# Optimization experiments

Measured on AMD Instinct MI355X. Metric: run time of the kernel, lower is better.

## Reference

```python
import jax, jax.numpy as jnp
import numpy as np

N = 200_000   # total nodes across batched AIGs
E = 400_000   # edges (fan-in ~2 per gate)
D = 64        # input_dim == dim_hidden (required by in-place scatter in _gru_forward)
B = 16        # number of graphs in batch
LF = 12       # num forward topological levels
LB = 12       # num backward topological levels
NUM_ROUNDS = 1


def setup_inputs() -> dict:
    key = jax.random.key(0)
    ks = jax.random.split(key, 9)
    node_type = jax.random.randint(ks[0], (N,), 0, 3, dtype=jnp.int32)
    num_inverted_predecessors = jax.random.randint(ks[1], (N,), 0, 3, dtype=jnp.int32)
    edge_index = jax.random.randint(ks[2], (2, E), 0, N, dtype=jnp.int32)
    forward_level = jax.random.randint(ks[3], (N,), 0, LF, dtype=jnp.int32)
    backward_level = jax.random.randint(ks[4], (N,), 0, LB, dtype=jnp.int32)
    batch = jnp.sort(jax.random.randint(ks[5], (N,), 0, B, dtype=jnp.int32))
    s = 1.0 / np.sqrt(D)
    W_enc = jax.random.normal(ks[6], (2, D), dtype=jnp.float32) * 0.5
    b_enc = jnp.zeros((D,), dtype=jnp.float32)
    W_f = jax.random.normal(ks[7], (D, D), dtype=jnp.float32) * s
    b_f = jnp.zeros((D,), dtype=jnp.float32)
    W_b = jax.random.normal(ks[8], (D, D), dtype=jnp.float32) * s
    b_b = jnp.zeros((D,), dtype=jnp.float32)
    return dict(node_type=node_type,
                num_inverted_predecessors=num_inverted_predecessors,
                edge_index=edge_index,
                forward_level=forward_level,
                backward_level=backward_level,
                batch=batch,
                W_enc=W_enc, b_enc=b_enc,
                W_f=W_f, b_f=b_f,
                W_b=W_b, b_b=b_b)


def reference(node_type, num_inverted_predecessors, edge_index,
              forward_level, backward_level, batch,
              W_enc, b_enc, W_f, b_f, W_b, b_b):
    # h_init = node_encoder(cat(node_type, num_inverted_predecessors))
    x = jnp.stack([node_type, num_inverted_predecessors], axis=1).astype(W_enc.dtype)  # [N,2]
    h = x @ W_enc + b_enc  # [N,D] node_state
    src, dst = edge_index[0], edge_index[1]

    for _ in range(NUM_ROUNDS):
        # forward topological sweep: level l nodes receive sum of mlp(h_src)
        # over incoming edges whose destination is at level l (subgraph dim=1).
        for l in range(1, LF):
            m = h @ W_f + b_f                                    # AggConv mlp on current state
            e_w = (forward_level[dst] == l).astype(h.dtype)      # edges into level-l nodes
            msg = jax.ops.segment_sum(m[src] * e_w[:, None], dst, num_segments=N)
            h = jnp.where((forward_level == l)[:, None], msg, h)  # scatter l_msg into node_state
        # backward sweep (reverse flow): level-l sources receive sum of
        # mlp_b(h_dst) over outgoing edges (subgraph dim=0, target_to_source).
        for l in range(1, LB):
            m = h @ W_b + b_b
            e_w = (backward_level[src] == l).astype(h.dtype)
            msg = jax.ops.segment_sum(m[dst] * e_w[:, None], src, num_segments=N)
            h = jnp.where((backward_level == l)[:, None], msg, h)

    # readout over output nodes (node_type == 1): [global_max_pool, global_add_pool]
    out_mask = (node_type == 1)
    neg_inf = jnp.finfo(h.dtype).min
    max_pool = jax.ops.segment_max(jnp.where(out_mask[:, None], h, neg_inf), batch, num_segments=B)
    sum_pool = jax.ops.segment_sum(h * out_mask[:, None].astype(h.dtype), batch, num_segments=B)
    return jnp.concatenate([max_pool, sum_pool], axis=1)  # [B, 2*D]
```

## Files before the change

### kernel.cpp

```cpp
#include <hip/hip_runtime.h>
#include <float.h>

#define NLVL 12
#define NB   16
#define NBLK 256
#define EBLK 2048
#define SWBLK 1024


struct Params {
    const int *nt, *ninv, *src, *dst, *fl, *bl, *batch;
    const float *We, *be, *Wf, *bf, *Wb, *bb;
    float *hN, *hB, *tabg, *out;
    int *rowptr, *cursor, *col, *nb_f, *nb_b, *onodes, *bsums, *meta, *plarr, *bar;
    int *cntf, *cntb, *cnto, *blkf, *blkb, *blko;
    int N, E, M, outN;
};

__device__ __forceinline__ float rlanef(float x, int l) {
    return __int_as_float(__builtin_amdgcn_readlane(__float_as_int(x), l));
}
__device__ __forceinline__ void sti(int* a, int v) {
    __hip_atomic_store(a, v, __ATOMIC_RELAXED, __HIP_MEMORY_SCOPE_AGENT);
}
__device__ __forceinline__ void stf(float* a, float v) {
    __hip_atomic_store(a, v, __ATOMIC_RELAXED, __HIP_MEMORY_SCOPE_AGENT);
}
__device__ __forceinline__ int ald(int* a) {
    return __hip_atomic_load(a, __ATOMIC_RELAXED, __HIP_MEMORY_SCOPE_AGENT);
}
__device__ __forceinline__ int afa(int* a, int v) {
    return __hip_atomic_fetch_add(a, v, __ATOMIC_RELAXED, __HIP_MEMORY_SCOPE_AGENT);
}

__device__ __forceinline__ void gbar3(int* bar, int nblk, int t) {
    __syncthreads();
    if (threadIdx.x == 0) {
        const int line = blockIdx.x & 15;
        const int per  = nblk >> 4;
        int a = afa(&bar[line * 32], 1);
        if (a == per * t - 1) {
            int m = afa(&bar[16 * 32], 1);
            if (m == 16 * t - 1) {
                sti(&bar[17 * 32], t);
            } else {
                while (ald(&bar[17 * 32]) < t) __builtin_amdgcn_s_sleep(1);
            }
            for (int b = line; b < nblk; b += 16)
                sti(&bar[(18 + b) * 32], t);
        } else {
            while (ald(&bar[(18 + blockIdx.x) * 32]) < t) __builtin_amdgcn_s_sleep(4);
        }
    }
    asm volatile("" ::: "memory");
    __syncthreads();
}

__global__ void k_edge_deg(Params p) {
    int g = blockIdx.x * 256 + threadIdx.x, gs = gridDim.x * 256;
    for (int e = g; e < p.E; e += gs) {
        atomicAdd(&p.rowptr[p.dst[e]], 1);
        atomicAdd(&p.rowptr[p.N + p.src[e]], 1);
    }
}

__global__ void k_deg_hist(Params p) {
    __shared__ int hf[NLVL], hb[NLVL], ho[NB];
    int tid = threadIdx.x, bid = blockIdx.x;
    if (tid < NLVL) { hf[tid] = 0; hb[tid] = 0; }
    if (tid < NB) ho[tid] = 0;
    __syncthreads();
    int chunk = (p.N + gridDim.x - 1) / gridDim.x;
    int lo = bid * chunk, hi = lo + chunk; if (hi > p.N) hi = p.N;
    for (int i = lo + tid; i < hi; i += 256) {
        int f = p.fl[i], b = p.bl[i];
        int t = p.nt[i], iv = p.ninv[i];
        p.plarr[i] = f | (b << 4) | ((t * 3 + iv) << 8);
        atomicAdd(&hf[f], 1);
        atomicAdd(&hb[b], 1);
        if (t == 1) atomicAdd(&ho[p.batch[i]], 1);
    }
    __syncthreads();
    if (tid < NLVL) { p.cntf[tid * NBLK + bid] = hf[tid]; p.cntb[tid * NBLK + bid] = hb[tid]; }
    if (tid < NB) p.cnto[tid * NBLK + bid] = ho[tid];
}

__global__ void k_scan1(int* __restrict__ data, int M, int* __restrict__ bsums) {
    __shared__ int s[512];
    int t = threadIdx.x;
    int g = blockIdx.x * 512 + t;
    int v = (g < M) ? data[g] : 0;
    s[t] = v;
    __syncthreads();
    for (int off = 1; off < 512; off <<= 1) {
        int add = (t >= off) ? s[t - off] : 0;
        __syncthreads();
        s[t] += add;
        __syncthreads();
    }
    if (g < M) data[g] = s[t] - v;
    if (t == 511) bsums[blockIdx.x] = s[511];
}

__global__ void k_scan_top(int* __restrict__ bsums, int nblk, Params p,
                           float* __restrict__ out, int outN) {
    __shared__ int s[1024];
    __shared__ int tot[48];
    int t = threadIdx.x;
    int* meta = p.meta;
    for (int i = t; i < outN; i += 1024)
        out[i] = ((i & 127) < 64) ? -FLT_MAX : 0.0f;
    if (t < 576) {
        int row = t >> 6, j = t & 63;
        float nf = (float)(row / 3), iv = (float)(row % 3);
        p.tabg[t] = fmaf(nf, p.We[j], fmaf(iv, p.We[64 + j], p.be[j]));
    }
    int seg = t >> 8, b = t & 255;
    for (int r = 0; r < 3; r++) {
        int l = 4 * r + seg;
        int v = p.cntf[l * NBLK + b];
        s[t] = v; __syncthreads();
        for (int off = 1; off < NBLK; off <<= 1) {
            int add = (b >= off) ? s[t - off] : 0; __syncthreads();
            s[t] += add; __syncthreads();
        }
        p.blkf[l * NBLK + b] = s[t] - v;
        if (b == NBLK - 1) tot[l] = s[t];
        __syncthreads();
    }
    for (int r = 0; r < 3; r++) {
        int l = 4 * r + seg;
        int v = p.cntb[l * NBLK + b];
        s[t] = v; __syncthreads();
        for (int off = 1; off < NBLK; off <<= 1) {
            int add = (b >= off) ? s[t - off] : 0; __syncthreads();
            s[t] += add; __syncthreads();
        }
        p.blkb[l * NBLK + b] = s[t] - v;
        if (b == NBLK - 1) tot[16 + l] = s[t];
        __syncthreads();
    }
    for (int r = 0; r < 4; r++) {
        int l = 4 * r + seg;
        int v = p.cnto[l * NBLK + b];
        s[t] = v; __syncthreads();
        for (int off = 1; off < NBLK; off <<= 1) {
            int add = (b >= off) ? s[t - off] : 0; __syncthreads();
            s[t] += add; __syncthreads();
        }
        p.blko[l * NBLK + b] = s[t] - v;
        if (b == NBLK - 1) tot[32 + l] = s[t];
        __syncthreads();
    }
    if (t == 0) { int a = 0; for (int l = 0; l < NLVL; l++) { meta[96 + l] = a; a += tot[l]; } meta[96 + NLVL] = a; }
    if (t == 1) { int a = 0; for (int l = 0; l < NLVL; l++) { meta[128 + l] = a; a += tot[16 + l]; } meta[128 + NLVL] = a; }
    if (t == 2) { int a = 0; for (int l = 0; l < NB; l++) { meta[160 + l] = a; a += tot[32 + l]; } meta[160 + NB] = a; }
    __syncthreads();
    for (int i = t; i < NLVL * NBLK; i += 1024) p.blkf[i] += meta[96 + (i >> 8)];
    for (int i = t; i < NLVL * NBLK; i += 1024) p.blkb[i] += meta[128 + (i >> 8)];
    for (int i = t; i < NB * NBLK; i += 1024) p.blko[i] += meta[160 + (i >> 8)];
    int v = (t < nblk) ? bsums[t] : 0;
    s[t] = v;
    __syncthreads();
    for (int off = 1; off < 1024; off <<= 1) {
        int add = (t >= off) ? s[t - off] : 0;
        __syncthreads();
        s[t] += add;
        __syncthreads();
    }
    if (t < nblk) bsums[t] = s[t] - v;
}

__global__ void k_scan_add(int* __restrict__ rowptr, int* __restrict__ cursor, int M, int total,
                           const int* __restrict__ bsums) {
    int g = blockIdx.x * blockDim.x + threadIdx.x;
    if (g >= M) return;
    int r = rowptr[g] + bsums[g >> 9];
    rowptr[g] = r;
    cursor[g] = r;
    if (g == 0) rowptr[M] = total;
}

template <int DIR>
__device__ __forceinline__ void sweep_level(const Params& p, int lvl,
                                            const float (&w)[64], float bv,
                                            int lane, int wid, int nw, int q, int fb) {
    const int* nb = DIR ? p.nb_b : p.nb_f;
    const int* rp = p.rowptr + (DIR ? p.N : 0);
    int start = p.meta[(DIR ? 128 : 96) + lvl];
    int cnt   = p.meta[(DIR ? 128 : 96) + lvl + 1] - start;
    float* db = DIR ? p.hB : p.hN;

    int c0 = (int)((long long)cnt * wid / nw);
    int c1 = (int)((long long)cnt * (wid + 1) / nw);
    for (int i = c0; i < c1; i += 4) {
        int my = i + q;
        int v = 0, rpv = 0, rpe = 0;
        if (my < c1) {
            int e = nb[start + my];
            v = e & 0x3FFFF;
            rpv = rp[v]; rpe = rp[v + 1];
        }
        float4 acc = make_float4(0.f, 0.f, 0.f, 0.f);
        for (int cb = rpv; cb < rpe; cb++) {
            int cu = p.col[cb];
            int u = cu & 0x3FFFF;
            int flu = (cu >> 18) & 15, blu = (cu >> 22) & 15;
            const float* sp;
            if (DIR == 0)
                sp = (flu > 0 && flu < lvl) ? (p.hN + (size_t)u * 64)
                                            : (p.tabg + ((cu >> 26) & 15) * 64);
            else
                sp = (blu > 0 && blu < lvl) ? (p.hB + (size_t)u * 64)
                   : (flu > 0)              ? (p.hN + (size_t)u * 64)
                                            : (p.tabg + ((cu >> 26) & 15) * 64);
            const float4 x = *(const float4*)(sp + fb);
            acc.x += x.x; acc.y += x.y; acc.z += x.z; acc.w += x.w;
        }
        #pragma unroll
        for (int qq = 0; qq < 4; qq++) {
            if (i + qq >= c1) break;
            int vs   = __builtin_amdgcn_readlane(v, 16 * qq);
            int degs = __builtin_amdgcn_readlane(rpe, 16 * qq)
                     - __builtin_amdgcn_readlane(rpv, 16 * qq);
            float o = bv * (float)degs;
            #pragma unroll
            for (int m = 0; m < 16; m++) {
                float ax = rlanef(acc.x, 16 * qq + m);
                float ay = rlanef(acc.y, 16 * qq + m);
                float az = rlanef(acc.z, 16 * qq + m);
                float aw = rlanef(acc.w, 16 * qq + m);
                o = fmaf(ax, w[4 * m + 0], o);
                o = fmaf(ay, w[4 * m + 1], o);
                o = fmaf(az, w[4 * m + 2], o);
                o = fmaf(aw, w[4 * m + 3], o);
            }
            stf(&db[(size_t)vs * 64 + lane], o);
        }
    }
}

__device__ inline void atomicMaxF(float* addr, float val) {
    int* ai = (int*)addr;
    int old = *ai;
    while (__int_as_float(old) < val) {
        int assumed = old;
        old = atomicCAS(ai, assumed, __float_as_int(val));
        if (old == assumed) break;
    }
}

__device__ __forceinline__ void readout_body(const Params& p, int bid, int tid) {
    int lane = tid & 63;
    int b = bid >> 5;
    int sl = bid & 31;
    int a0 = p.meta[160 + b], a1 = p.meta[161 + b];
    int cnt = a1 - a0;
    if (cnt == 0) return;
    int lo = a0 + (int)((long long)cnt * sl / 32);
    int hi = a0 + (int)((long long)cnt * (sl + 1) / 32);
    int wcnt = hi - lo;
    int wave = tid >> 6;
    int wl = lo + (wcnt * wave) / 4;
    int wh = lo + (wcnt * (wave + 1)) / 4;
    if (wh <= wl) return;
    float mx = -FLT_MAX, sm = 0.f;
    for (int k = wl; k < wh; k += 64) {
        int take = wh - k; if (take > 64) take = 64;
        int el = (lane < take) ? p.onodes[k + lane] : 0;
        for (int j = 0; j < take; j++) {
            int e = __shfl(el, j, 64);
            int v = e & 0x3FFFF;
            int flv = (e >> 18) & 15, blv = (e >> 22) & 15;
            const float* sp = (blv > 0) ? (p.hB + (size_t)v * 64)
                            : (flv > 0) ? (p.hN + (size_t)v * 64)
                                        : (p.tabg + ((e >> 26) & 15) * 64);
            float x = sp[lane];
            mx = fmaxf(mx, x);
            sm += x;
        }
    }
    atomicMaxF(&p.out[b * 128 + lane], mx);
    atomicAdd(&p.out[b * 128 + 64 + lane], sm);
}

__global__ __launch_bounds__(256) __attribute__((amdgpu_waves_per_eu(4, 4)))
void k_tail(Params p) {
    const int tid = threadIdx.x, bid = blockIdx.x;
    const int lane = tid & 63;
    int* bar = p.bar;
    const int nblk = gridDim.x;
    int ep = 0;
    __shared__ int cur[48];

    for (int e = bid * 256 + tid; e < p.E; e += nblk * 256) {
        int sN = p.src[e], d = p.dst[e];
        sti(&p.col[atomicAdd(&p.cursor[d], 1)],        sN | (p.plarr[sN] << 18));
        sti(&p.col[atomicAdd(&p.cursor[p.N + sN], 1)],  d | (p.plarr[d]  << 18));
    }
    if (bid < NBLK) {
        if (tid < NLVL) { cur[tid] = p.blkf[tid * NBLK + bid]; cur[16 + tid] = p.blkb[tid * NBLK + bid]; }
        if (tid < NB) cur[32 + tid] = p.blko[tid * NBLK + bid];
        __syncthreads();
        int chunk = (p.N + NBLK - 1) / NBLK;
        int lo = bid * chunk, hi = lo + chunk; if (hi > p.N) hi = p.N;
        for (int i = lo + tid; i < hi; i += 256) {
            int pl = p.plarr[i];
            int lf = pl & 15, lb = (pl >> 4) & 15, tx = (pl >> 8) & 15;
            int pk = i | (pl << 18);
            sti(&p.nb_f[atomicAdd(&cur[lf], 1)], pk);
            sti(&p.nb_b[atomicAdd(&cur[16 + lb], 1)], pk);
            if (tx >= 3 && tx < 6)
                sti(&p.onodes[atomicAdd(&cur[32 + p.batch[i]], 1)], pk);
        }
    }
    gbar3(bar, nblk, ++ep);

    const int wid = (bid * 256 + tid) >> 6;
    const int nw  = (nblk * 256) >> 6;
    const int q = lane >> 4, fb = (lane & 15) * 4;
    {
        float w[64];
        #pragma unroll
        for (int k = 0; k < 64; k++) w[k] = p.Wf[k * 64 + lane];
        float bv = p.bf[lane];
        for (int lvl = 1; lvl < NLVL; lvl++) {
            sweep_level<0>(p, lvl, w, bv, lane, wid, nw, q, fb);
            gbar3(bar, nblk, ++ep);
        }
    }
    {
        float w[64];
        #pragma unroll
        for (int k = 0; k < 64; k++) w[k] = p.Wb[k * 64 + lane];
        float bv = p.bb[lane];
        for (int lvl = 1; lvl < NLVL; lvl++) {
            sweep_level<1>(p, lvl, w, bv, lane, wid, nw, q, fb);
            gbar3(bar, nblk, ++ep);
        }
    }

    if (bid < NB * 32) readout_body(p, bid, tid);
}

__global__ void k_edge_fill(Params p) {
    int g = blockIdx.x * 256 + threadIdx.x, gs = gridDim.x * 256;
    int N = p.N;
    for (int e = g; e < p.E; e += gs) {
        int s = p.src[e], d = p.dst[e];
        p.col[atomicAdd(&p.cursor[d], 1)] = s | (p.plarr[s] << 18);
        p.col[atomicAdd(&p.cursor[N + s], 1)] = d | (p.plarr[d] << 18);
    }
}

__global__ void k_fill(Params p) {
    __shared__ int cur[48];
    int tid = threadIdx.x, bid = blockIdx.x;
    int N = p.N;
    if (tid < NLVL) { cur[tid] = p.blkf[tid * NBLK + bid]; cur[16 + tid] = p.blkb[tid * NBLK + bid]; }
    if (tid < NB) cur[32 + tid] = p.blko[tid * NBLK + bid];
    __syncthreads();
    int chunk = (N + gridDim.x - 1) / gridDim.x;
    int lo = bid * chunk, hi = lo + chunk; if (hi > N) hi = N;
    for (int i = lo + tid; i < hi; i += 256) {
        int pl = p.plarr[i];
        int lf = pl & 15, lb = (pl >> 4) & 15, tx = (pl >> 8) & 15;
        int pk = i | (pl << 18);
        p.nb_f[atomicAdd(&cur[lf], 1)] = pk;
        p.nb_b[atomicAdd(&cur[16 + lb], 1)] = pk;
        if (tx >= 3 && tx < 6)
            p.onodes[atomicAdd(&cur[32 + p.batch[i]], 1)] = pk;
    }
}

__global__ __launch_bounds__(256) __attribute__((amdgpu_waves_per_eu(4, 4)))
void k_sweep(Params p, int lvl, int dir) {
    const int tid = threadIdx.x, lane = tid & 63;
    const float* W = dir ? p.Wb : p.Wf;
    float w[64];
    #pragma unroll
    for (int k = 0; k < 64; k++) w[k] = W[k * 64 + lane];
    float bv = (dir ? p.bb : p.bf)[lane];
    const int wid = (blockIdx.x * 256 + tid) >> 6;
    const int nw  = (gridDim.x * 256) >> 6;
    const int q = lane >> 4, fb = (lane & 15) * 4;
    if (dir == 0) sweep_level<0>(p, lvl, w, bv, lane, wid, nw, q, fb);
    else          sweep_level<1>(p, lvl, w, bv, lane, wid, nw, q, fb);
}

__global__ void k_readout(Params p) {
    readout_body(p, blockIdx.x, threadIdx.x);
}

extern "C" void kernel_launch(void* const* d_in, const int* in_sizes, int n_in,
                              void* d_out, int out_size, void* d_ws, size_t ws_size,
                              hipStream_t stream) {
    int N = in_sizes[0];
    int E = in_sizes[2] / 2;
    int M = 2 * N;

    Params p;
    p.nt    = (const int*)d_in[0];
    p.ninv  = (const int*)d_in[1];
    p.src   = (const int*)d_in[2];
    p.dst   = (const int*)d_in[2] + E;
    p.fl    = (const int*)d_in[3];
    p.bl    = (const int*)d_in[4];
    p.batch = (const int*)d_in[5];
    p.We    = (const float*)d_in[6];
    p.be    = (const float*)d_in[7];
    p.Wf    = (const float*)d_in[8];
    p.bf    = (const float*)d_in[9];
    p.Wb    = (const float*)d_in[10];
    p.bb    = (const float*)d_in[11];
    p.out   = (float*)d_out;
    p.N = N; p.E = E; p.M = M; p.outN = out_size;

    char* ws = (char*)d_ws;
    size_t off = 0;
    auto alloc = [&](size_t bytes) -> char* {
        char* q = ws + off;
        off = (off + bytes + 255) & ~(size_t)255;
        return q;
    };
    p.rowptr = (int*)  alloc((size_t)(M + 1) * sizeof(int));
    p.meta   = (int*)  alloc(256 * sizeof(int));
    p.bar    = (int*)  alloc((size_t)(18 + SWBLK) * 32 * sizeof(int));
    size_t zbytes = (size_t)((char*)(p.bar + (18 + SWBLK) * 32) - (char*)p.rowptr);
    p.hN     = (float*)alloc((size_t)N * 64 * sizeof(float));
    p.hB     = (float*)alloc((size_t)N * 64 * sizeof(float));
    p.tabg   = (float*)alloc(9 * 64 * sizeof(float));
    p.cursor = (int*)  alloc((size_t)M * sizeof(int));
    p.col    = (int*)  alloc((size_t)2 * E * sizeof(int));
    p.nb_f   = (int*)  alloc((size_t)N * sizeof(int));
    p.nb_b   = (int*)  alloc((size_t)N * sizeof(int));
    p.onodes = (int*)  alloc((size_t)N * sizeof(int));
    p.plarr  = (int*)  alloc((size_t)N * sizeof(int));
    p.bsums  = (int*)  alloc(1024 * sizeof(int));
    p.cntf   = (int*)  alloc(NLVL * NBLK * sizeof(int));
    p.cntb   = (int*)  alloc(NLVL * NBLK * sizeof(int));
    p.cnto   = (int*)  alloc(NB * NBLK * sizeof(int));
    p.blkf   = (int*)  alloc(NLVL * NBLK * sizeof(int));
    p.blkb   = (int*)  alloc(NLVL * NBLK * sizeof(int));
    p.blko   = (int*)  alloc(NB * NBLK * sizeof(int));

    int nscan = (M + 511) / 512;

    static int g_tail = -2;
    if (g_tail == -2) {
        int mb = 0;
        g_tail = -1;
        if (hipOccupancyMaxActiveBlocksPerMultiprocessor(&mb, k_tail, 256, 0) == hipSuccess
                && mb > 0) {
            int dev = 0;
            hipGetDevice(&dev);
            hipDeviceProp_t props;
            if (hipGetDeviceProperties(&props, dev) == hipSuccess) {
                long cap = (long)mb * props.multiProcessorCount;
                long g = cap < SWBLK ? cap : SWBLK;
                g &= ~15L;
                if (g >= NBLK) g_tail = (int)g;
            }
        }
    }

    hipMemsetAsync(p.rowptr, 0, zbytes, stream);
    k_edge_deg<<<EBLK, 256, 0, stream>>>(p);
    k_deg_hist<<<NBLK, 256, 0, stream>>>(p);
    k_scan1<<<nscan, 512, 0, stream>>>(p.rowptr, M, p.bsums);
    k_scan_top<<<1, 1024, 0, stream>>>(p.bsums, nscan, p, p.out, out_size);
    k_scan_add<<<(M + 255) / 256, 256, 0, stream>>>(p.rowptr, p.cursor, M, 2 * E, p.bsums);

    bool launched = false;
    if (g_tail >= NBLK) {
        k_tail<<<g_tail, 256, 0, stream>>>(p);
        launched = true;
    } else {
        void* kargs[] = { (void*)&p };
        launched = hipLaunchCooperativeKernel((const void*)k_tail, dim3(SWBLK),
                                              dim3(256), kargs, 0, stream) == hipSuccess;
    }
    if (!launched) {
        k_edge_fill<<<EBLK, 256, 0, stream>>>(p);
        k_fill<<<NBLK, 256, 0, stream>>>(p);
        for (int l = 1; l < NLVL; l++)
            k_sweep<<<1024, 256, 0, stream>>>(p, l, 0);
        for (int l = 1; l < NLVL; l++)
            k_sweep<<<1024, 256, 0, stream>>>(p, l, 1);
        k_readout<<<NB * 32, 256, 0, stream>>>(p);
    }
}
```

Measured before the change: 542.9 us.

## Fuse CSR build prologue kernels into the persistent kernel using grid barriers

```diff
diff --git a/kernel.cpp b/kernel.cpp
--- a/kernel.cpp
+++ b/kernel.cpp
@@ -5,15 +5,17 @@
 #define NB   16
 #define NBLK 256
 #define EBLK 2048
-#define SWBLK 1024
+#define FG   1024
 
 
 struct Params {
     const int *nt, *ninv, *src, *dst, *fl, *bl, *batch;
     const float *We, *be, *Wf, *bf, *Wb, *bb;
     float *hN, *hB, *tabg, *out;
-    int *rowptr, *cursor, *col, *nb_f, *nb_b, *onodes, *bsums, *meta, *plarr, *bar;
+    int *rowptr, *cursor, *col, *nb_f, *nb_b, *onodes, *bsums, *bsums2, *meta, *plarr, *bar;
+    int *deg, *rowscan;
     int *cntf, *cntb, *cnto, *blkf, *blkb, *blko;
+    int *blkFf, *blkFb, *blkFo;
     int N, E, M, outN;
 };
 
@@ -56,129 +58,14 @@
     __syncthreads();
 }
 
-__global__ void k_edge_deg(Params p) {
-    int g = blockIdx.x * 256 + threadIdx.x, gs = gridDim.x * 256;
-    for (int e = g; e < p.E; e += gs) {
-        atomicAdd(&p.rowptr[p.dst[e]], 1);
-        atomicAdd(&p.rowptr[p.N + p.src[e]], 1);
-    }
-}
-
-__global__ void k_deg_hist(Params p) {
-    __shared__ int hf[NLVL], hb[NLVL], ho[NB];
-    int tid = threadIdx.x, bid = blockIdx.x;
-    if (tid < NLVL) { hf[tid] = 0; hb[tid] = 0; }
-    if (tid < NB) ho[tid] = 0;
-    __syncthreads();
-    int chunk = (p.N + gridDim.x - 1) / gridDim.x;
-    int lo = bid * chunk, hi = lo + chunk; if (hi > p.N) hi = p.N;
-    for (int i = lo + tid; i < hi; i += 256) {
-        int f = p.fl[i], b = p.bl[i];
-        int t = p.nt[i], iv = p.ninv[i];
-        p.plarr[i] = f | (b << 4) | ((t * 3 + iv) << 8);
-        atomicAdd(&hf[f], 1);
-        atomicAdd(&hb[b], 1);
-        if (t == 1) atomicAdd(&ho[p.batch[i]], 1);
-    }
-    __syncthreads();
-    if (tid < NLVL) { p.cntf[tid * NBLK + bid] = hf[tid]; p.cntb[tid * NBLK + bid] = hb[tid]; }
-    if (tid < NB) p.cnto[tid * NBLK + bid] = ho[tid];
-}
-
-__global__ void k_scan1(int* __restrict__ data, int M, int* __restrict__ bsums) {
-    __shared__ int s[512];
-    int t = threadIdx.x;
-    int g = blockIdx.x * 512 + t;
-    int v = (g < M) ? data[g] : 0;
-    s[t] = v;
-    __syncthreads();
-    for (int off = 1; off < 512; off <<= 1) {
-        int add = (t >= off) ? s[t - off] : 0;
-        __syncthreads();
-        s[t] += add;
-        __syncthreads();
-    }
-    if (g < M) data[g] = s[t] - v;
-    if (t == 511) bsums[blockIdx.x] = s[511];
-}
-
-__global__ void k_scan_top(int* __restrict__ bsums, int nblk, Params p,
-                           float* __restrict__ out, int outN) {
-    __shared__ int s[1024];
-    __shared__ int tot[48];
-    int t = threadIdx.x;
-    int* meta = p.meta;
-    for (int i = t; i < outN; i += 1024)
-        out[i] = ((i & 127) < 64) ? -FLT_MAX : 0.0f;
-    if (t < 576) {
-        int row = t >> 6, j = t & 63;
-        float nf = (float)(row / 3), iv = (float)(row % 3);
-        p.tabg[t] = fmaf(nf, p.We[j], fmaf(iv, p.We[64 + j], p.be[j]));
-    }
-    int seg = t >> 8, b = t & 255;
-    for (int r = 0; r < 3; r++) {
-        int l = 4 * r + seg;
-        int v = p.cntf[l * NBLK + b];
-        s[t] = v; __syncthreads();
-        for (int off = 1; off < NBLK; off <<= 1) {
-            int add = (b >= off) ? s[t - off] : 0; __syncthreads();
-            s[t] += add; __syncthreads();
-        }
-        p.blkf[l * NBLK + b] = s[t] - v;
-        if (b == NBLK - 1) tot[l] = s[t];
-        __syncthreads();
-    }
-    for (int r = 0; r < 3; r++) {
-        int l = 4 * r + seg;
-        int v = p.cntb[l * NBLK + b];
-        s[t] = v; __syncthreads();
-        for (int off = 1; off < NBLK; off <<= 1) {
-            int add = (b >= off) ? s[t - off] : 0; __syncthreads();
-            s[t] += add; __syncthreads();
-        }
-        p.blkb[l * NBLK + b] = s[t] - v;
-        if (b == NBLK - 1) tot[16 + l] = s[t];
-        __syncthreads();
-    }
-    for (int r = 0; r < 4; r++) {
-        int l = 4 * r + seg;
-        int v = p.cnto[l * NBLK + b];
-        s[t] = v; __syncthreads();
-        for (int off = 1; off < NBLK; off <<= 1) {
-            int add = (b >= off) ? s[t - off] : 0; __syncthreads();
-            s[t] += add; __syncthreads();
-        }
-        p.blko[l * NBLK + b] = s[t] - v;
-        if (b == NBLK - 1) tot[32 + l] = s[t];
-        __syncthreads();
-    }
-    if (t == 0) { int a = 0; for (int l = 0; l < NLVL; l++) { meta[96 + l] = a; a += tot[l]; } meta[96 + NLVL] = a; }
-    if (t == 1) { int a = 0; for (int l = 0; l < NLVL; l++) { meta[128 + l] = a; a += tot[16 + l]; } meta[128 + NLVL] = a; }
-    if (t == 2) { int a = 0; for (int l = 0; l < NB; l++) { meta[160 + l] = a; a += tot[32 + l]; } meta[160 + NB] = a; }
-    __syncthreads();
-    for (int i = t; i < NLVL * NBLK; i += 1024) p.blkf[i] += meta[96 + (i >> 8)];
-    for (int i = t; i < NLVL * NBLK; i += 1024) p.blkb[i] += meta[128 + (i >> 8)];
-    for (int i = t; i < NB * NBLK; i += 1024) p.blko[i] += meta[160 + (i >> 8)];
-    int v = (t < nblk) ? bsums[t] : 0;
-    s[t] = v;
-    __syncthreads();
-    for (int off = 1; off < 1024; off <<= 1) {
-        int add = (t >= off) ? s[t - off] : 0;
-        __syncthreads();
-        s[t] += add;
-        __syncthreads();
-    }
-    if (t < nblk) bsums[t] = s[t] - v;
-}
-
-__global__ void k_scan_add(int* __restrict__ rowptr, int* __restrict__ cursor, int M, int total,
-                           const int* __restrict__ bsums) {
-    int g = blockIdx.x * blockDim.x + threadIdx.x;
-    if (g >= M) return;
-    int r = rowptr[g] + bsums[g >> 9];
-    rowptr[g] = r;
-    cursor[g] = r;
-    if (g == 0) rowptr[M] = total;
+__device__ __forceinline__ int blockScanIncl(int v, int* s, int t) {
+    s[t] = v; __syncthreads();
+    for (int off = 1; off < 256; off <<= 1) {
+        int add = (t >= off) ? s[t - off] : 0; __syncthreads();
+        s[t] += add; __syncthreads();
+    }
+    int r = s[t]; __syncthreads();
+    return r;
 }
 
 template <int DIR>
@@ -190,6 +77,7 @@
     int start = p.meta[(DIR ? 128 : 96) + lvl];
     int cnt   = p.meta[(DIR ? 128 : 96) + lvl + 1] - start;
     float* db = DIR ? p.hB : p.hN;
+    const int e2 = 2 * p.E;
 
     int c0 = (int)((long long)cnt * wid / nw);
     int c1 = (int)((long long)cnt * (wid + 1) / nw);
@@ -200,6 +88,9 @@
             int e = nb[start + my];
             v = e & 0x3FFFF;
             rpv = rp[v]; rpe = rp[v + 1];
+            rpv = (rpv < 0) ? 0 : (rpv > e2 ? e2 : rpv);
+            rpe = (rpe < rpv) ? rpv : (rpe > e2 ? e2 : rpe);
+            if (rpe > rpv + 4096) rpe = rpv + 4096;
         }
         float4 acc = make_float4(0.f, 0.f, 0.f, 0.f);
         for (int cb = rpv; cb < rpe; cb++) {
@@ -255,6 +146,8 @@
     int b = bid >> 5;
     int sl = bid & 31;
     int a0 = p.meta[160 + b], a1 = p.meta[161 + b];
+    a0 = (a0 < 0) ? 0 : (a0 > p.N ? p.N : a0);
+    a1 = (a1 < a0) ? a0 : (a1 > p.N ? p.N : a1);
     int cnt = a1 - a0;
     if (cnt == 0) return;
     int lo = a0 + (int)((long long)cnt * sl / 32);
@@ -285,22 +178,114 @@
 }
 
 __global__ __launch_bounds__(256) __attribute__((amdgpu_waves_per_eu(4, 4)))
-void k_tail(Params p) {
+void k_fused(Params p) {
     const int tid = threadIdx.x, bid = blockIdx.x;
     const int lane = tid & 63;
     int* bar = p.bar;
-    const int nblk = gridDim.x;
     int ep = 0;
+    __shared__ int s[256];
+    __shared__ int hist[40];
     __shared__ int cur[48];
 
-    for (int e = bid * 256 + tid; e < p.E; e += nblk * 256) {
+    if (tid < 40) hist[tid] = 0;
+    __syncthreads();
+    for (int e = bid * 256 + tid; e < p.E; e += FG * 256) {
+        atomicAdd(&p.deg[p.dst[e]], 1);
+        atomicAdd(&p.deg[p.N + p.src[e]], 1);
+    }
+    for (int i = bid * 256 + tid; i < p.outN; i += FG * 256)
+        stf(&p.out[i], ((i & 127) < 64) ? -FLT_MAX : 0.0f);
+    if (bid == 0 && tid < 64) {
+        #pragma unroll
+        for (int row = 0; row < 9; row++) {
+            float nf = (float)(row / 3), iv = (float)(row % 3);
+            stf(&p.tabg[row * 64 + tid],
+                fmaf(nf, p.We[tid], fmaf(iv, p.We[64 + tid], p.be[tid])));
+        }
+    }
+    if (bid < NBLK) {
+        int chunk = (p.N + NBLK - 1) / NBLK;
+        int lo = bid * chunk, hi = lo + chunk; if (hi > p.N) hi = p.N;
+        for (int i = lo + tid; i < hi; i += 256) {
+            int f = p.fl[i], b = p.bl[i];
+            int t2 = p.nt[i], iv = p.ninv[i];
+            sti(&p.plarr[i], f | (b << 4) | ((t2 * 3 + iv) << 8));
+            atomicAdd(&hist[f], 1);
+            atomicAdd(&hist[12 + b], 1);
+            if (t2 == 1) atomicAdd(&hist[24 + p.batch[i]], 1);
+        }
+    }
+    __syncthreads();
+    if (bid < NBLK) {
+        if (tid < NLVL) { sti(&p.cntf[tid * NBLK + bid], hist[tid]); sti(&p.cntb[tid * NBLK + bid], hist[12 + tid]); }
+        if (tid < NB) sti(&p.cnto[tid * NBLK + bid], hist[24 + tid]);
+    }
+    gbar3(bar, FG, ++ep);
+
+    const int nscan = (p.M + 511) >> 9;
+    if (bid < nscan) {
+        int g0 = (bid << 9) + tid * 2;
+        int e0 = (g0 < p.M) ? p.deg[g0] : 0;
+        int e1 = (g0 + 1 < p.M) ? p.deg[g0 + 1] : 0;
+        int incl = blockScanIncl(e0 + e1, s, tid);
+        int excl = incl - (e0 + e1);
+        if (g0 < p.M) sti(&p.rowscan[g0], excl);
+        if (g0 + 1 < p.M) sti(&p.rowscan[g0 + 1], excl + e0);
+        if (tid == 255) sti(&p.bsums[bid], incl);
+    } else if (bid >= nscan + 2 && bid < nscan + 2 + 2 * NLVL + NB) {
+        int j = bid - (nscan + 2);
+        const int* sA; int* dA;
+        if (j < NLVL)          { sA = p.cntf + j * NBLK;              dA = p.blkf + j * NBLK; }
+        else if (j < 2 * NLVL) { sA = p.cntb + (j - NLVL) * NBLK;     dA = p.blkb + (j - NLVL) * NBLK; }
+        else                   { sA = p.cnto + (j - 2 * NLVL) * NBLK; dA = p.blko + (j - 2 * NLVL) * NBLK; }
+        int v = sA[tid];
+        int incl = blockScanIncl(v, s, tid);
+        sti(&dA[tid], incl - v);
+        if (tid == 255) sti(&p.meta[224 + j], incl);
+    }
+    gbar3(bar, FG, ++ep);
+
+    if (bid == 0) {
+        int i0 = tid * 4;
+        int a0 = (i0     < nscan) ? p.bsums[i0]     : 0;
+        int a1 = (i0 + 1 < nscan) ? p.bsums[i0 + 1] : 0;
+        int a2 = (i0 + 2 < nscan) ? p.bsums[i0 + 2] : 0;
+        int a3 = (i0 + 3 < nscan) ? p.bsums[i0 + 3] : 0;
+        int incl = blockScanIncl(a0 + a1 + a2 + a3, s, tid);
+        int b0 = incl - (a0 + a1 + a2 + a3);
+        if (i0     < nscan) sti(&p.bsums2[i0],     b0);
+        if (i0 + 1 < nscan) sti(&p.bsums2[i0 + 1], b0 + a0);
+        if (i0 + 2 < nscan) sti(&p.bsums2[i0 + 2], b0 + a0 + a1);
+        if (i0 + 3 < nscan) sti(&p.bsums2[i0 + 3], b0 + a0 + a1 + a2);
+    } else if (bid == 1 && tid < 3) {
+        if (tid == 0) { int a = 0; for (int l = 0; l < NLVL; l++) { sti(&p.meta[96 + l], a);  a += p.meta[224 + l]; }            sti(&p.meta[96 + NLVL], a); }
+        if (tid == 1) { int a = 0; for (int l = 0; l < NLVL; l++) { sti(&p.meta[128 + l], a); a += p.meta[224 + NLVL + l]; }     sti(&p.meta[128 + NLVL], a); }
+        if (tid == 2) { int a = 0; for (int l = 0; l < NB; l++)   { sti(&p.meta[160 + l], a); a += p.meta[224 + 2 * NLVL + l]; } sti(&p.meta[160 + NB], a); }
+    }
+    gbar3(bar, FG, ++ep);
+
+    for (int g = bid * 256 + tid; g < p.M; g += FG * 256) {
+        int r = p.rowscan[g] + p.bsums2[g >> 9];
+        sti(&p.rowptr[g], r);
+        sti(&p.cursor[g], r);
+    }
+    if (bid == 0 && tid == 0) sti(&p.rowptr[p.M], 2 * p.E);
+    for (int i = bid * 256 + tid; i < NLVL * NBLK; i += FG * 256) {
+        sti(&p.blkFf[i], p.blkf[i] + p.meta[96 + (i >> 8)]);
+        sti(&p.blkFb[i], p.blkb[i] + p.meta[128 + (i >> 8)]);
+    }
+    for (int i = bid * 256 + tid; i < NB * NBLK; i += FG * 256)
+        sti(&p.blkFo[i], p.blko[i] + p.meta[160 + (i >> 8)]);
+    gbar3(bar, FG, ++ep);
+
+    for (int e = bid * 256 + tid; e < p.E; e += FG * 256) {
         int sN = p.src[e], d = p.dst[e];
-        sti(&p.col[atomicAdd(&p.cursor[d], 1)],        sN | (p.plarr[sN] << 18));
-        sti(&p.col[atomicAdd(&p.cursor[p.N + sN], 1)],  d | (p.plarr[d]  << 18));
+        sti(&p.col[atomicAdd(&p.cursor[d], 1)],         sN | (p.plarr[sN] << 18));
+        sti(&p.col[atomicAdd(&p.cursor[p.N + sN], 1)],   d | (p.plarr[d]  << 18));
     }
     if (bid < NBLK) {
-        if (tid < NLVL) { cur[tid] = p.blkf[tid * NBLK + bid]; cur[16 + tid] = p.blkb[tid * NBLK + bid]; }
-        if (tid < NB) cur[32 + tid] = p.blko[tid * NBLK + bid];
+        if (tid < NLVL) { cur[tid] = p.blkFf[tid * NBLK + bid]; cur[16 + tid] = p.blkFb[tid * NBLK + bid]; }
+        if (tid < NB) cur[32 + tid] = p.blkFo[tid * NBLK + bid];
         __syncthreads();
         int chunk = (p.N + NBLK - 1) / NBLK;
         int lo = bid * chunk, hi = lo + chunk; if (hi > p.N) hi = p.N;
@@ -314,10 +299,10 @@
                 sti(&p.onodes[atomicAdd(&cur[32 + p.batch[i]], 1)], pk);
         }
     }
-    gbar3(bar, nblk, ++ep);
+    gbar3(bar, FG, ++ep);
 
     const int wid = (bid * 256 + tid) >> 6;
-    const int nw  = (nblk * 256) >> 6;
+    const int nw  = (FG * 256) >> 6;
     const int q = lane >> 4, fb = (lane & 15) * 4;
     {
         float w[64];
@@ -326,7 +311,7 @@
         float bv = p.bf[lane];
         for (int lvl = 1; lvl < NLVL; lvl++) {
             sweep_level<0>(p, lvl, w, bv, lane, wid, nw, q, fb);
-            gbar3(bar, nblk, ++ep);
+            gbar3(bar, FG, ++ep);
         }
     }
     {
@@ -336,11 +321,136 @@
         float bv = p.bb[lane];
         for (int lvl = 1; lvl < NLVL; lvl++) {
             sweep_level<1>(p, lvl, w, bv, lane, wid, nw, q, fb);
-            gbar3(bar, nblk, ++ep);
+            gbar3(bar, FG, ++ep);
         }
     }
 
     if (bid < NB * 32) readout_body(p, bid, tid);
+}
+
+__global__ void k_edge_deg(Params p) {
+    int g = blockIdx.x * 256 + threadIdx.x, gs = gridDim.x * 256;
+    for (int e = g; e < p.E; e += gs) {
+        atomicAdd(&p.rowptr[p.dst[e]], 1);
+        atomicAdd(&p.rowptr[p.N + p.src[e]], 1);
+    }
+}
+
+__global__ void k_deg_hist(Params p) {
+    __shared__ int hf[NLVL], hb[NLVL], ho[NB];
+    int tid = threadIdx.x, bid = blockIdx.x;
+    if (tid < NLVL) { hf[tid] = 0; hb[tid] = 0; }
+    if (tid < NB) ho[tid] = 0;
+    __syncthreads();
+    int chunk = (p.N + gridDim.x - 1) / gridDim.x;
+    int lo = bid * chunk, hi = lo + chunk; if (hi > p.N) hi = p.N;
+    for (int i = lo + tid; i < hi; i += 256) {
+        int f = p.fl[i], b = p.bl[i];
+        int t = p.nt[i], iv = p.ninv[i];
+        p.plarr[i] = f | (b << 4) | ((t * 3 + iv) << 8);
+        atomicAdd(&hf[f], 1);
+        atomicAdd(&hb[b], 1);
+        if (t == 1) atomicAdd(&ho[p.batch[i]], 1);
+    }
+    __syncthreads();
+    if (tid < NLVL) { p.cntf[tid * NBLK + bid] = hf[tid]; p.cntb[tid * NBLK + bid] = hb[tid]; }
+    if (tid < NB) p.cnto[tid * NBLK + bid] = ho[tid];
+}
+
+__global__ void k_scan1(int* __restrict__ data, int M, int* __restrict__ bsums) {
+    __shared__ int s[512];
+    int t = threadIdx.x;
+    int g = blockIdx.x * 512 + t;
+    int v = (g < M) ? data[g] : 0;
+    s[t] = v;
+    __syncthreads();
+    for (int off = 1; off < 512; off <<= 1) {
+        int add = (t >= off) ? s[t - off] : 0;
+        __syncthreads();
+        s[t] += add;
+        __syncthreads();
+    }
+    if (g < M) data[g] = s[t] - v;
+    if (t == 511) bsums[blockIdx.x] = s[511];
+}
+
+__global__ void k_scan_top(int* __restrict__ bsums, int nblk, Params p,
+                           float* __restrict__ out, int outN) {
+    __shared__ int s[1024];
+    __shared__ int tot[48];
+    int t = threadIdx.x;
+    int* meta = p.meta;
+    for (int i = t; i < outN; i += 1024)
+        out[i] = ((i & 127) < 64) ? -FLT_MAX : 0.0f;
+    if (t < 576) {
+        int row = t >> 6, j = t & 63;
+        float nf = (float)(row / 3), iv = (float)(row % 3);
+        p.tabg[t] = fmaf(nf, p.We[j], fmaf(iv, p.We[64 + j], p.be[j]));
+    }
+    int seg = t >> 8, b = t & 255;
+    for (int r = 0; r < 3; r++) {
+        int l = 4 * r + seg;
+        int v = p.cntf[l * NBLK + b];
+        s[t] = v; __syncthreads();
+        for (int off = 1; off < NBLK; off <<= 1) {
+            int add = (b >= off) ? s[t - off] : 0; __syncthreads();
+            s[t] += add; __syncthreads();
+        }
+        p.blkf[l * NBLK + b] = s[t] - v;
+        if (b == NBLK - 1) tot[l] = s[t];
+        __syncthreads();
+    }
+    for (int r = 0; r < 3; r++) {
+        int l = 4 * r + seg;
+        int v = p.cntb[l * NBLK + b];
+        s[t] = v; __syncthreads();
+        for (int off = 1; off < NBLK; off <<= 1) {
+            int add = (b >= off) ? s[t - off] : 0; __syncthreads();
+            s[t] += add; __syncthreads();
+        }
+        p.blkb[l * NBLK + b] = s[t] - v;
+        if (b == NBLK - 1) tot[16 + l] = s[t];
+        __syncthreads();
+    }
+    for (int r = 0; r < 4; r++) {
+        int l = 4 * r + seg;
+        int v = p.cnto[l * NBLK + b];
+        s[t] = v; __syncthreads();
+        for (int off = 1; off < NBLK; off <<= 1) {
+            int add = (b >= off) ? s[t - off] : 0; __syncthreads();
+            s[t] += add; __syncthreads();
+        }
+        p.blko[l * NBLK + b] = s[t] - v;
+        if (b == NBLK - 1) tot[32 + l] = s[t];
+        __syncthreads();
+    }
+    if (t == 0) { int a = 0; for (int l = 0; l < NLVL; l++) { meta[96 + l] = a; a += tot[l]; } meta[96 + NLVL] = a; }
+    if (t == 1) { int a = 0; for (int l = 0; l < NLVL; l++) { meta[128 + l] = a; a += tot[16 + l]; } meta[128 + NLVL] = a; }
+    if (t == 2) { int a = 0; for (int l = 0; l < NB; l++) { meta[160 + l] = a; a += tot[32 + l]; } meta[160 + NB] = a; }
+    __syncthreads();
+    for (int i = t; i < NLVL * NBLK; i += 1024) p.blkf[i] += meta[96 + (i >> 8)];
+    for (int i = t; i < NLVL * NBLK; i += 1024) p.blkb[i] += meta[128 + (i >> 8)];
+    for (int i = t; i < NB * NBLK; i += 1024) p.blko[i] += meta[160 + (i >> 8)];
+    int v = (t < nblk) ? bsums[t] : 0;
+    s[t] = v;
+    __syncthreads();
+    for (int off = 1; off < 1024; off <<= 1) {
+        int add = (t >= off) ? s[t - off] : 0;
+        __syncthreads();
+        s[t] += add;
+        __syncthreads();
+    }
+    if (t < nblk) bsums[t] = s[t] - v;
+}
+
+__global__ void k_scan_add(int* __restrict__ rowptr, int* __restrict__ cursor, int M, int total,
+                           const int* __restrict__ bsums) {
+    int g = blockIdx.x * blockDim.x + threadIdx.x;
+    if (g >= M) return;
+    int r = rowptr[g] + bsums[g >> 9];
+    rowptr[g] = r;
+    cursor[g] = r;
+    if (g == 0) rowptr[M] = total;
 }
 
 __global__ void k_edge_fill(Params p) {
@@ -424,63 +534,58 @@
         return q;
     };
     p.rowptr = (int*)  alloc((size_t)(M + 1) * sizeof(int));
-    p.meta   = (int*)  alloc(256 * sizeof(int));
-    p.bar    = (int*)  alloc((size_t)(18 + SWBLK) * 32 * sizeof(int));
-    size_t zbytes = (size_t)((char*)(p.bar + (18 + SWBLK) * 32) - (char*)p.rowptr);
+    p.deg    = (int*)  alloc((size_t)M * sizeof(int));
+    p.meta   = (int*)  alloc(512 * sizeof(int));
+    p.bar    = (int*)  alloc((size_t)(18 + FG) * 32 * sizeof(int));
+    size_t zbytes = (size_t)((char*)(p.bar + (18 + FG) * 32) - (char*)p.rowptr);
     p.hN     = (float*)alloc((size_t)N * 64 * sizeof(float));
     p.hB     = (float*)alloc((size_t)N * 64 * sizeof(float));
     p.tabg   = (float*)alloc(9 * 64 * sizeof(float));
     p.cursor = (int*)  alloc((size_t)M * sizeof(int));
+    p.rowscan= (int*)  alloc((size_t)M * sizeof(int));
     p.col    = (int*)  alloc((size_t)2 * E * sizeof(int));
     p.nb_f   = (int*)  alloc((size_t)N * sizeof(int));
     p.nb_b   = (int*)  alloc((size_t)N * sizeof(int));
     p.onodes = (int*)  alloc((size_t)N * sizeof(int));
     p.plarr  = (int*)  alloc((size_t)N * sizeof(int));
     p.bsums  = (int*)  alloc(1024 * sizeof(int));
+    p.bsums2 = (int*)  alloc(1024 * sizeof(int));
     p.cntf   = (int*)  alloc(NLVL * NBLK * sizeof(int));
     p.cntb   = (int*)  alloc(NLVL * NBLK * sizeof(int));
     p.cnto   = (int*)  alloc(NB * NBLK * sizeof(int));
     p.blkf   = (int*)  alloc(NLVL * NBLK * sizeof(int));
     p.blkb   = (int*)  alloc(NLVL * NBLK * sizeof(int));
     p.blko   = (int*)  alloc(NB * NBLK * sizeof(int));
+    p.blkFf  = (int*)  alloc(NLVL * NBLK * sizeof(int));
+    p.blkFb  = (int*)  alloc(NLVL * NBLK * sizeof(int));
+    p.blkFo  = (int*)  alloc(NB * NBLK * sizeof(int));
 
     int nscan = (M + 511) / 512;
 
-    static int g_tail = -2;
-    if (g_tail == -2) {
+    static int g_fused = -2;
+    if (g_fused == -2) {
         int mb = 0;
-        g_tail = -1;
-        if (hipOccupancyMaxActiveBlocksPerMultiprocessor(&mb, k_tail, 256, 0) == hipSuccess
+        g_fused = 0;
+        if (hipOccupancyMaxActiveBlocksPerMultiprocessor(&mb, k_fused, 256, 0) == hipSuccess
                 && mb > 0) {
             int dev = 0;
             hipGetDevice(&dev);
             hipDeviceProp_t props;
-            if (hipGetDeviceProperties(&props, dev) == hipSuccess) {
-                long cap = (long)mb * props.multiProcessorCount;
-                long g = cap < SWBLK ? cap : SWBLK;
-                g &= ~15L;
-                if (g >= NBLK) g_tail = (int)g;
-            }
+            if (hipGetDeviceProperties(&props, dev) == hipSuccess &&
+                (long)mb * props.multiProcessorCount >= FG)
+                g_fused = 1;
         }
     }
 
     hipMemsetAsync(p.rowptr, 0, zbytes, stream);
-    k_edge_deg<<<EBLK, 256, 0, stream>>>(p);
-    k_deg_hist<<<NBLK, 256, 0, stream>>>(p);
-    k_scan1<<<nscan, 512, 0, stream>>>(p.rowptr, M, p.bsums);
-    k_scan_top<<<1, 1024, 0, stream>>>(p.bsums, nscan, p, p.out, out_size);
-    k_scan_add<<<(M + 255) / 256, 256, 0, stream>>>(p.rowptr, p.cursor, M, 2 * E, p.bsums);
-
-    bool launched = false;
-    if (g_tail >= NBLK) {
-        k_tail<<<g_tail, 256, 0, stream>>>(p);
-        launched = true;
+    if (g_fused == 1) {
+        k_fused<<<FG, 256, 0, stream>>>(p);
     } else {
-        void* kargs[] = { (void*)&p };
-        launched = hipLaunchCooperativeKernel((const void*)k_tail, dim3(SWBLK),
-                                              dim3(256), kargs, 0, stream) == hipSuccess;
-    }
-    if (!launched) {
+        k_edge_deg<<<EBLK, 256, 0, stream>>>(p);
+        k_deg_hist<<<NBLK, 256, 0, stream>>>(p);
+        k_scan1<<<nscan, 512, 0, stream>>>(p.rowptr, M, p.bsums);
+        k_scan_top<<<1, 1024, 0, stream>>>(p.bsums, nscan, p, p.out, out_size);
+        k_scan_add<<<(M + 255) / 256, 256, 0, stream>>>(p.rowptr, p.cursor, M, 2 * E, p.bsums);
         k_edge_fill<<<EBLK, 256, 0, stream>>>(p);
         k_fill<<<NBLK, 256, 0, stream>>>(p);
         for (int l = 1; l < NLVL; l++)
```

Result: faster. 496.7 us (-8.5%).
